# Kernel tuning notes

Hardware: AMD Instinct MI355X
Metric: run time of the kernel (lower is better)

Reference implementation:

```python
import jax, jax.numpy as jnp
import numpy as np

SEQ_LEN = 4096
EMBED_DIM = 1280
NUM_HEADS = 16
HEAD_DIM = EMBED_DIM // NUM_HEADS  # 80
SCALING = float(np.sqrt(HEAD_DIM))  # NOTE: source multiplies by sqrt(head_dim)
NEG_INF = float(np.finfo(np.float32).min)


def rotate_half(x):
    x1, x2 = jnp.split(x, 2, axis=-1)
    return jnp.concatenate((-x2, x1), axis=-1)


def setup_inputs() -> dict:
    key = jax.random.key(0)
    ks = jax.random.split(key, 7)
    s = 0.02
    hidden_states = jax.random.normal(ks[0], (SEQ_LEN, EMBED_DIM), dtype=jnp.float32)
    w_qkv = jax.random.normal(ks[1], (3 * EMBED_DIM, EMBED_DIM), dtype=jnp.float32) * s
    b_qkv = jax.random.normal(ks[2], (3 * EMBED_DIM,), dtype=jnp.float32) * s
    w_proj = jax.random.normal(ks[3], (EMBED_DIM, EMBED_DIM), dtype=jnp.float32) * s
    b_proj = jax.random.normal(ks[4], (EMBED_DIM,), dtype=jnp.float32) * s
    # rotary angles: theta duplicated to head_dim (emb = cat(rope, rope))
    inv_freq = 1.0 / (10000.0 ** (jnp.arange(0, HEAD_DIM // 2, dtype=jnp.float32) * 2.0 / HEAD_DIM))
    pos = jnp.arange(SEQ_LEN, dtype=jnp.float32)
    freqs = pos[:, None] * inv_freq[None, :]            # [S, hd/2]
    emb = jnp.concatenate((freqs, freqs), axis=-1)       # [S, hd]
    cos = jnp.cos(emb)
    sin = jnp.sin(emb)
    # 4 packed images of 1024 patches each
    cu_seqlens = jnp.array([0, 1024, 2048, 3072, 4096], dtype=jnp.int32)
    return {
        "hidden_states": hidden_states,
        "w_qkv": w_qkv, "b_qkv": b_qkv,
        "w_proj": w_proj, "b_proj": b_proj,
        "cos": cos, "sin": sin,
        "cu_seqlens": cu_seqlens,
    }


def reference(hidden_states, w_qkv, b_qkv, w_proj, b_proj, cos, sin, cu_seqlens):
    S = hidden_states.shape[0]
    # packed QKV projection
    qkv = hidden_states @ w_qkv.T + b_qkv                  # [S, 3D]
    qkv = qkv.reshape(S, 3, NUM_HEADS, HEAD_DIM)
    q, k, v = qkv[:, 0], qkv[:, 1], qkv[:, 2]              # [S, H, hd]
    # fp32 RoPE (broadcast cos/sin over heads)
    c = cos[:, None, :].astype(jnp.float32)
    sn = sin[:, None, :].astype(jnp.float32)
    qf, kf = q.astype(jnp.float32), k.astype(jnp.float32)
    q = (qf * c + rotate_half(qf) * sn).astype(q.dtype)
    k = (kf * c + rotate_half(kf) * sn).astype(k.dtype)
    # block-diagonal mask from cu_seqlens: same segment -> 0, else -inf
    pos = jnp.arange(S)
    seg = jnp.searchsorted(cu_seqlens, pos, side="right") - 1  # [S]
    bias = jnp.where(seg[:, None] == seg[None, :], 0.0, NEG_INF)  # [S, S]
    # dense attention over whole packed sequence (as in source)
    scores = jnp.einsum("shd,thd->hst", q, k) * SCALING + bias[None]
    weights = jax.nn.softmax(scores.astype(jnp.float32), axis=-1).astype(q.dtype)
    attn = jnp.einsum("hst,thd->shd", weights, v).reshape(S, EMBED_DIM)
    return attn @ w_proj.T + b_proj
```

## Files before the change

### kernel.cpp

```cpp
#include <hip/hip_runtime.h>

#define SEQ   4096
#define EMB   1280
#define NH    16
#define HD    80
#define HDP   96
#define O3    3840
#define SEGLEN 1024
#define NSEG  4
#define QSCALE (8.94427190999915878564f * 1.44269504088896340736f)

typedef unsigned short u16;
typedef __attribute__((ext_vector_type(8))) _Float16 f16x8;
typedef __attribute__((ext_vector_type(4))) _Float16 f16x4;
typedef __attribute__((ext_vector_type(2))) __fp16   h16x2;
typedef __attribute__((ext_vector_type(4))) float    f32x4;

__device__ __forceinline__ float ex2(float x) { return __builtin_amdgcn_exp2f(x); }

__device__ __forceinline__ u16 f2h(float f) {
  union { _Float16 h; u16 u; } v; v.h = (_Float16)f; return v.u;
}
__device__ __forceinline__ float h2f(u16 b) {
  union { u16 u; _Float16 h; } v; v.u = b; return (float)v.h;
}
__device__ __forceinline__ f32x4 exp2_4(f32x4 x) {
  f32x4 r; r.x = ex2(x.x); r.y = ex2(x.y); r.z = ex2(x.z); r.w = ex2(x.w); return r;
}
__device__ __forceinline__ f16x4 pk4(f32x4 s) {
  union { h16x2 h[2]; f16x4 f; } u;
  u.h[0] = __builtin_amdgcn_cvt_pkrtz(s.x, s.y);
  u.h[1] = __builtin_amdgcn_cvt_pkrtz(s.z, s.w);
  return u.f;
}
__device__ __forceinline__ void gl2lds16(const u16* g, u16* l) {
  __builtin_amdgcn_global_load_lds(
      (const __attribute__((address_space(1))) unsigned int*)g,
      (__attribute__((address_space(3))) unsigned int*)l, 16, 0, 0);
}

#define CVT_N1 (SEQ * EMB / 4)
#define CVT_N2 (O3 * EMB / 4)
#define CVT_N3 (EMB * EMB / 4)
__global__ void cvt_all_kernel(const float* __restrict__ a, const float* __restrict__ b,
                               const float* __restrict__ c, u16* __restrict__ oa,
                               u16* __restrict__ ob, u16* __restrict__ oc) {
  int i = blockIdx.x * blockDim.x + threadIdx.x;
  const float* src; u16* dst; int j = i;
  if (j < CVT_N1)                { src = a; dst = oa; }
  else if (j < CVT_N1 + CVT_N2)  { src = b; dst = ob; j -= CVT_N1; }
  else                           { src = c; dst = oc; j -= CVT_N1 + CVT_N2; }
  float4 f = ((const float4*)src)[j];
  union { u16 h[4]; uint2 v; } o;
  o.h[0] = f2h(f.x); o.h[1] = f2h(f.y); o.h[2] = f2h(f.z); o.h[3] = f2h(f.w);
  ((uint2*)dst)[j] = o.v;
}

template<int OUTF>
__global__ __launch_bounds__(256)
void gemm_bias_kernel(const u16* __restrict__ A, const u16* __restrict__ W,
                      const float* __restrict__ bias, void* __restrict__ Cout,
                      int N, int K) {
  __shared__ u16 As[128][64];
  __shared__ u16 Bs[128][64];
  const int tid  = threadIdx.x;
  const int flat = blockIdx.x + gridDim.x * blockIdx.y;
  const int cpx  = (gridDim.x * gridDim.y) >> 3;
  const int nid  = (flat & 7) * cpx + (flat >> 3);
  const int bm   = nid / gridDim.x, bn = nid % gridDim.x;
  const int lane = tid & 63;
  const int wid  = tid >> 6;
  const int wm   = (wid >> 1) * 64, wn = (wid & 1) * 64;
  const int lr   = lane & 15, quad = lane >> 4;

  f32x4 acc[4][4];
  const f32x4 z4 = {0.f, 0.f, 0.f, 0.f};
  #pragma unroll
  for (int i = 0; i < 4; ++i)
    #pragma unroll
    for (int j = 0; j < 4; ++j) acc[i][j] = z4;

  const int arow = tid >> 3;
  const int acol = (((tid & 7) ^ (arow & 7)) * 8);
  const u16* Ab = A + (size_t)(bm * 128) * K;
  const u16* Wb = W + (size_t)(bn * 128) * K;
  u16* AsL = &As[0][0] + tid * 8;
  u16* BsL = &Bs[0][0] + tid * 8;

  for (int kt = 0; kt < K; kt += 64) {
    #pragma unroll
    for (int r = 0; r < 4; ++r) {
      gl2lds16(&Ab[(size_t)(arow + r * 32) * K + kt + acol], AsL + r * 2048);
      gl2lds16(&Wb[(size_t)(arow + r * 32) * K + kt + acol], BsL + r * 2048);
    }
    __syncthreads();
    #pragma unroll
    for (int k32 = 0; k32 < 2; ++k32) {
      const int c = (((k32 * 4 + quad) ^ (lr & 7)) * 8);
      f16x8 aF[4], bF[4];
      #pragma unroll
      for (int i = 0; i < 4; ++i) {
        aF[i] = *(const f16x8*)&As[wm + i * 16 + lr][c];
        bF[i] = *(const f16x8*)&Bs[wn + i * 16 + lr][c];
      }
      #pragma unroll
      for (int i = 0; i < 4; ++i)
        #pragma unroll
        for (int j = 0; j < 4; ++j)
          acc[i][j] = __builtin_amdgcn_mfma_f32_16x16x32_f16(aF[i], bF[j], acc[i][j], 0, 0, 0);
    }
    __syncthreads();
  }

  #pragma unroll
  for (int i = 0; i < 4; ++i) {
    int rowb = bm * 128 + wm + i * 16 + quad * 4;
    #pragma unroll
    for (int j = 0; j < 4; ++j) {
      int col = bn * 128 + wn + j * 16 + lr;
      float bv = bias[col];
      #pragma unroll
      for (int r = 0; r < 4; ++r) {
        float v = acc[i][j][r] + bv;
        if (OUTF) ((float*)Cout)[(size_t)(rowb + r) * N + col] = v;
        else      ((u16*)Cout)[(size_t)(rowb + r) * N + col] = f2h(v);
      }
    }
  }
}

__global__ __launch_bounds__(512, 2)
void gemm256_kernel(const u16* __restrict__ A, const u16* __restrict__ W,
                    const float* __restrict__ bias, u16* __restrict__ Cout,
                    int N, int K) {
  __shared__ u16 As[2][256][64];
  __shared__ u16 Bs[2][256][64];
  const int tid  = threadIdx.x;
  const int flat = blockIdx.x + gridDim.x * blockIdx.y;
  const int cpx  = (gridDim.x * gridDim.y) >> 3;
  const int nid  = (flat & 7) * cpx + (flat >> 3);
  const int bm   = nid / gridDim.x, bn = nid % gridDim.x;
  const int lane = tid & 63;
  const int wid  = tid >> 6;
  const int wm   = wid >> 2;
  const int wn   = wid & 3;
  const int lr   = lane & 15, quad = lane >> 4;
  const int NT   = K >> 6;

  const u16* Ab = A + (size_t)(bm * 256) * K;
  const u16* Wb = W + (size_t)(bn * 256) * K;

  const int srr  = tid >> 3;
  const int scol = ((tid & 7) ^ (srr & 7)) << 3;
  const u16* ApL = Ab + (size_t)srr * K + scol;
  const u16* WpL = Wb + (size_t)srr * K + scol;

  auto stA = [&](int b, int row0, int t) {
    gl2lds16(ApL + (size_t)row0 * K + t * 64,        &As[b][row0][0]      + tid * 8);
    gl2lds16(ApL + (size_t)(row0 + 64) * K + t * 64, &As[b][row0 + 64][0] + tid * 8);
  };
  auto stB = [&](int b, int row0, int t) {
    gl2lds16(WpL + (size_t)row0 * K + t * 64,        &Bs[b][row0][0]      + tid * 8);
    gl2lds16(WpL + (size_t)(row0 + 64) * K + t * 64, &Bs[b][row0 + 64][0] + tid * 8);
  };

  f32x4 acc[8][4];
  const f32x4 z4 = {0.f, 0.f, 0.f, 0.f};
  #pragma unroll
  for (int i = 0; i < 8; ++i)
    #pragma unroll
    for (int j = 0; j < 4; ++j) acc[i][j] = z4;

  stA(0, 0, 0); stA(0, 128, 0);
  stB(0, 0, 0); stB(0, 128, 0);
  stA(1, 0, 1);
  asm volatile("s_waitcnt vmcnt(2)" ::: "memory");
  __builtin_amdgcn_s_barrier();

  for (int t = 0; t < NT; ++t) {
    const int buf = t & 1, nb = buf ^ 1;
    #pragma unroll
    for (int mq = 0; mq < 2; ++mq) {
      #pragma unroll
      for (int k32 = 0; k32 < 2; ++k32) {
        const int c = (((k32 * 4 + quad) ^ (lr & 7)) << 3);
        f16x8 aF[4], bF[4];
        #pragma unroll
        for (int i = 0; i < 4; ++i)
          aF[i] = *(const f16x8*)&As[buf][mq * 128 + wm * 64 + i * 16 + lr][c];
        #pragma unroll
        for (int j = 0; j < 4; ++j)
          bF[j] = *(const f16x8*)&Bs[buf][wn * 64 + j * 16 + lr][c];
        __builtin_amdgcn_sched_barrier(0);
        if (mq == 0 && k32 == 0) {
          if (t + 1 < NT) { stB(nb, 0, t + 1); stA(nb, 128, t + 1); }
        } else if (mq == 0 && k32 == 1) {
          if (t + 1 < NT) stB(nb, 128, t + 1);
        } else if (mq == 1 && k32 == 0) {
          if (t + 2 < NT) stA(buf, 0, t + 2);
        }
        __builtin_amdgcn_s_barrier();
        asm volatile("s_waitcnt lgkmcnt(0)" ::: "memory");
        __builtin_amdgcn_sched_barrier(0);
        __builtin_amdgcn_s_setprio(1);
        #pragma unroll
        for (int i = 0; i < 4; ++i)
          #pragma unroll
          for (int j = 0; j < 4; ++j)
            acc[mq * 4 + i][j] =
                __builtin_amdgcn_mfma_f32_16x16x32_f16(aF[i], bF[j], acc[mq * 4 + i][j], 0, 0, 0);
        __builtin_amdgcn_s_setprio(0);
        if (mq == 1 && k32 == 1) {
          if (t < NT - 2) asm volatile("s_waitcnt vmcnt(2)" ::: "memory");
          else            asm volatile("s_waitcnt vmcnt(0)" ::: "memory");
        }
        __builtin_amdgcn_s_barrier();
        __builtin_amdgcn_sched_barrier(0);
      }
    }
  }

  #pragma unroll
  for (int mq = 0; mq < 2; ++mq) {
    #pragma unroll
    for (int i = 0; i < 4; ++i) {
      const int rowb = bm * 256 + mq * 128 + wm * 64 + i * 16 + quad * 4;
      #pragma unroll
      for (int j = 0; j < 4; ++j) {
        const int col = bn * 256 + wn * 64 + j * 16 + lr;
        const float bv = bias[col];
        #pragma unroll
        for (int r = 0; r < 4; ++r)
          Cout[(size_t)(rowb + r) * N + col] = f2h(acc[mq * 4 + i][j][r] + bv);
      }
    }
  }
}

__global__ __launch_bounds__(256)
void rope_reorg_kernel(const u16* __restrict__ qkv, const float* __restrict__ cosp,
                       const float* __restrict__ sinp, u16* __restrict__ Qp,
                       u16* __restrict__ Kp, u16* __restrict__ Vt) {
  __shared__ u16 Qs[64][80];
  __shared__ u16 Ks[64][80];
  __shared__ u16 Vs[64][88];
  const int tid = threadIdx.x;
  const int s0 = blockIdx.x * 64;
  const int h  = blockIdx.y;

  for (int t = tid; t < 640; t += 256) {
    int r = t / 10, c = (t % 10) * 8;
    size_t g = (size_t)(s0 + r) * O3 + h * HD + c;
    *(uint4*)&Qs[r][c] = *(const uint4*)&qkv[g];
    *(uint4*)&Ks[r][c] = *(const uint4*)&qkv[g + EMB];
    *(uint4*)&Vs[r][c] = *(const uint4*)&qkv[g + 2 * EMB];
  }
  __syncthreads();

  for (int t = tid; t < 64 * 24; t += 256) {
    int r = t / 24, d4 = (t % 24) * 4;
    int s = s0 + r;
    size_t po = ((size_t)h * SEQ + s) * HDP + d4;
    if (d4 >= HD) {
      uint2 z = make_uint2(0, 0);
      *(uint2*)&Qp[po] = z; *(uint2*)&Kp[po] = z;
      continue;
    }
    float4 cv = *(const float4*)&cosp[(size_t)s * HD + d4];
    float4 sv = *(const float4*)&sinp[(size_t)s * HD + d4];
    int dp4 = (d4 < 40) ? d4 + 40 : d4 - 40;
    float sgn = (d4 < 40) ? -1.f : 1.f;
    union { u16 h[4]; uint2 v; } oq, ok;
    const float* cp = (const float*)&cv;
    const float* sp = (const float*)&sv;
    #pragma unroll
    for (int j = 0; j < 4; ++j) {
      float q  = h2f(Qs[r][d4 + j]),  k  = h2f(Ks[r][d4 + j]);
      float qp = h2f(Qs[r][dp4 + j]), kp = h2f(Ks[r][dp4 + j]);
      oq.h[j] = f2h((q * cp[j] + sgn * qp * sp[j]) * QSCALE);
      ok.h[j] = f2h(k * cp[j] + sgn * kp * sp[j]);
    }
    *(uint2*)&Qp[po] = oq.v;
    *(uint2*)&Kp[po] = ok.v;
  }

  for (int t = tid; t < HD * 8; t += 256) {
    int d = t / 8, sc = (t % 8) * 8;
    union { u16 h[8]; uint4 v; } o;
    #pragma unroll
    for (int j = 0; j < 8; ++j) o.h[j] = Vs[sc + j][d];
    *(uint4*)&Vt[((size_t)(h * HD + d)) * SEQ + s0 + sc] = o.v;
  }
}

__global__ __launch_bounds__(512)
void attn_kernel(const u16* __restrict__ Qp, const u16* __restrict__ Kp,
                 const u16* __restrict__ Vt, u16* __restrict__ attnO) {
  __shared__ u16 K_l[3][64][96];
  __shared__ u16 V_l[3][96][64];
  const int BUFSZ = 6144;

  const int tid = threadIdx.x;
  const int lane = tid & 63, w = tid >> 6;
  const int lr = lane & 15, quad = lane >> 4;
  const int flat = blockIdx.x + 8 * blockIdx.y + 128 * blockIdx.z;
  const int nid  = (flat & 7) * 64 + (flat >> 3);
  const int qb   = nid & 7;
  const int h    = (nid >> 3) & 15;
  const int sg   = nid >> 7;
  const int seg0 = sg * SEGLEN;
  const int q0b = seg0 + qb * 128;

  f16x8 qF[3];
  {
    int qrow = q0b + w * 16 + lr;
    #pragma unroll
    for (int kc = 0; kc < 3; ++kc)
      qF[kc] = *(const f16x8*)&Qp[((size_t)h * SEQ + qrow) * HDP + kc * 32 + quad * 8];
  }
  asm volatile("" :: "v"(qF[0]), "v"(qF[1]), "v"(qF[2]));
  asm volatile("s_waitcnt vmcnt(0)" ::: "memory");

  {
    u16 val = (tid < 32) ? (u16)0x3C00 : (u16)0;
    #pragma unroll
    for (int b = 0; b < 3; ++b) {
      u16* q = &V_l[0][0][0] + b * BUFSZ + 80 * 64 + tid * 2;
      q[0] = val; q[1] = val;
    }
  }

  const u16* Kbase = Kp + ((size_t)h * SEQ + seg0) * HDP;
  const u16* Vbase = Vt + (size_t)h * HD * SEQ + seg0;
  const u16* pG[3]; u16* dB[3]; int gAdv[3];
  #pragma unroll
  for (int t = 0; t < 3; ++t) {
    int s = t * 512 + tid;
    if (s < 768) {
      int r = s / 12, c = s % 12;
      int ck = (c & ~3) | ((c & 3) ^ ((r >> 1) & 3));
      pG[t] = Kbase + (size_t)r * HDP + ck * 8;
      dB[t] = &K_l[0][0][0] + s * 8;
      gAdv[t] = 64 * HDP;
    } else {
      int sv = (s < 1408) ? s - 768 : s - 1408;
      int rv = sv / 8, cv = sv % 8;
      int cg = cv ^ (rv & 7);
      pG[t] = Vbase + (size_t)rv * SEQ + cg * 8;
      dB[t] = &V_l[0][0][0] + sv * 8;
      gAdv[t] = 64;
    }
  }

  auto stage_adv = [&](int b) {
    #pragma unroll
    for (int t = 0; t < 3; ++t) {
      gl2lds16(pG[t], dB[t] + b * BUFSZ);
      pG[t] += gAdv[t];
    }
  };

  const f32x4 z4 = {0.f, 0.f, 0.f, 0.f};
  float m_r = -3.0e38f;
  f32x4 Oacc[6];
  #pragma unroll
  for (int n = 0; n < 6; ++n) Oacc[n] = z4;

  const int kswz = (lr >> 1) & 3;

  stage_adv(0);
  stage_adv(1);
  asm volatile("s_waitcnt vmcnt(3) lgkmcnt(0)" ::: "memory");
  __builtin_amdgcn_s_barrier();
  __builtin_amdgcn_sched_barrier(0);

  int buf = 0, sb = 2;
  for (int kt = 0; kt < SEGLEN; kt += 64) {
    if (kt + 128 < SEGLEN) stage_adv(sb);

    const u16* kb = &K_l[0][0][0] + buf * BUFSZ;
    const u16* vb = &V_l[0][0][0] + buf * BUFSZ;

    f32x4 S[4];
    __builtin_amdgcn_s_setprio(1);
    #pragma unroll
    for (int ct = 0; ct < 4; ++ct) {
      S[ct] = z4;
      #pragma unroll
      for (int kc = 0; kc < 3; ++kc) {
        f16x8 kF = *(const f16x8*)&kb[(ct * 16 + lr) * 96 + kc * 32 + ((quad ^ kswz) << 3)];
        S[ct] = __builtin_amdgcn_mfma_f32_16x16x32_f16(kF, qF[kc], S[ct], 0, 0, 0);
      }
    }
    __builtin_amdgcn_s_setprio(0);

    float mx = fmaxf(fmaxf(S[0].x, S[0].y), fmaxf(S[0].z, S[0].w));
    #pragma unroll
    for (int ct = 1; ct < 4; ++ct)
      mx = fmaxf(mx, fmaxf(fmaxf(S[ct].x, S[ct].y), fmaxf(S[ct].z, S[ct].w)));
    mx = fmaxf(mx, __shfl_xor(mx, 16, 64));
    mx = fmaxf(mx, __shfl_xor(mx, 32, 64));
    float mnew = fmaxf(m_r, mx);
    float alpha = ex2(m_r - mnew);
    m_r = mnew;

    f32x4 mv = {mnew, mnew, mnew, mnew};
    #pragma unroll
    for (int ct = 0; ct < 4; ++ct) S[ct] = exp2_4(S[ct] - mv);

    if (__ballot(alpha != 1.0f)) {
      f32x4 al;
      al.x = __shfl(alpha, quad * 4 + 0, 64);
      al.y = __shfl(alpha, quad * 4 + 1, 64);
      al.z = __shfl(alpha, quad * 4 + 2, 64);
      al.w = __shfl(alpha, quad * 4 + 3, 64);
      #pragma unroll
      for (int n = 0; n < 6; ++n) Oacc[n] *= al;
    }

    f16x4 pF[4];
    #pragma unroll
    for (int ct = 0; ct < 4; ++ct) pF[ct] = pk4(S[ct]);

    __builtin_amdgcn_s_setprio(1);
    #pragma unroll
    for (int ct = 0; ct < 4; ++ct) {
      const int cchunk = 2 * ct + (quad >> 1);
      #pragma unroll
      for (int n = 0; n < 6; ++n) {
        int vrow = n * 16 + lr;
        const u16* vp = vb + vrow * 64 + ((cchunk ^ (vrow & 7)) << 3) + ((quad & 1) << 2);
        f16x4 vF = *(const f16x4*)vp;
        Oacc[n] = __builtin_amdgcn_mfma_f32_16x16x16f16(pF[ct], vF, Oacc[n], 0, 0, 0);
      }
    }
    __builtin_amdgcn_s_setprio(0);

    if (kt + 128 < SEGLEN) asm volatile("s_waitcnt vmcnt(3)" ::: "memory");
    else                   asm volatile("s_waitcnt vmcnt(0)" ::: "memory");
    __builtin_amdgcn_s_barrier();
    __builtin_amdgcn_sched_barrier(0);

    buf = (buf == 2) ? 0 : buf + 1;
    sb  = (sb == 2) ? 0 : sb + 1;
  }

  f32x4 linv;
  linv.x = 1.0f / __shfl(Oacc[5].x, quad << 4, 64);
  linv.y = 1.0f / __shfl(Oacc[5].y, quad << 4, 64);
  linv.z = 1.0f / __shfl(Oacc[5].z, quad << 4, 64);
  linv.w = 1.0f / __shfl(Oacc[5].w, quad << 4, 64);
  #pragma unroll
  for (int n = 0; n < 5; ++n) {
    int rowb = q0b + w * 16 + quad * 4;
    int col = h * HD + n * 16 + lr;
    attnO[(size_t)(rowb + 0) * EMB + col] = f2h(Oacc[n].x * linv.x);
    attnO[(size_t)(rowb + 1) * EMB + col] = f2h(Oacc[n].y * linv.y);
    attnO[(size_t)(rowb + 2) * EMB + col] = f2h(Oacc[n].z * linv.z);
    attnO[(size_t)(rowb + 3) * EMB + col] = f2h(Oacc[n].w * linv.w);
  }
}

extern "C" void kernel_launch(void* const* d_in, const int* in_sizes, int n_in,
                              void* d_out, int out_size, void* d_ws, size_t ws_size,
                              hipStream_t stream) {
  const float* hs     = (const float*)d_in[0];
  const float* w_qkv  = (const float*)d_in[1];
  const float* b_qkv  = (const float*)d_in[2];
  const float* w_proj = (const float*)d_in[3];
  const float* b_proj = (const float*)d_in[4];
  const float* cosp   = (const float*)d_in[5];
  const float* sinp   = (const float*)d_in[6];
  float* out = (float*)d_out;

  char* p = (char*)d_ws;
  auto take = [&](size_t bytes) { char* q = p; p += (bytes + 255) & ~(size_t)255; return q; };
  u16* hsH    = (u16*)take((size_t)SEQ * EMB * 2);
  u16* wqkvH  = (u16*)take((size_t)O3 * EMB * 2);
  u16* wprojH = (u16*)take((size_t)EMB * EMB * 2);
  u16* qkvO   = (u16*)take((size_t)SEQ * O3 * 2);
  u16* Qp     = (u16*)take((size_t)NH * SEQ * HDP * 2);
  u16* Kp     = (u16*)take((size_t)NH * SEQ * HDP * 2);
  u16* Vt     = (u16*)take((size_t)NH * HD * SEQ * 2);
  u16* attnH  = (u16*)take((size_t)SEQ * EMB * 2);

  int ncvt = (CVT_N1 + CVT_N2 + CVT_N3) / 256;
  cvt_all_kernel<<<ncvt, 256, 0, stream>>>(hs, w_qkv, w_proj, hsH, wqkvH, wprojH);

  gemm256_kernel<<<dim3(O3 / 256, SEQ / 256), 512, 0, stream>>>(hsH, wqkvH, b_qkv, qkvO, O3, EMB);

  rope_reorg_kernel<<<dim3(SEQ / 64, NH), 256, 0, stream>>>(qkvO, cosp, sinp, Qp, Kp, Vt);

  attn_kernel<<<dim3(SEGLEN / 128, NH, NSEG), 512, 0, stream>>>(Qp, Kp, Vt, attnH);

  gemm_bias_kernel<1><<<dim3(EMB / 128, SEQ / 128), 256, 0, stream>>>(attnH, wprojH, b_proj, out, EMB, EMB);
}
```

Baseline: 233.5 us.

## Simplify GEMM pipeline to whole-tile double buffering with one barrier per K-step

```diff
diff --git a/kernel.cpp b/kernel.cpp
--- a/kernel.cpp
+++ b/kernel.cpp
@@ -155,13 +155,13 @@
   const u16* ApL = Ab + (size_t)srr * K + scol;
   const u16* WpL = Wb + (size_t)srr * K + scol;
 
-  auto stA = [&](int b, int row0, int t) {
-    gl2lds16(ApL + (size_t)row0 * K + t * 64,        &As[b][row0][0]      + tid * 8);
-    gl2lds16(ApL + (size_t)(row0 + 64) * K + t * 64, &As[b][row0 + 64][0] + tid * 8);
-  };
-  auto stB = [&](int b, int row0, int t) {
-    gl2lds16(WpL + (size_t)row0 * K + t * 64,        &Bs[b][row0][0]      + tid * 8);
-    gl2lds16(WpL + (size_t)(row0 + 64) * K + t * 64, &Bs[b][row0 + 64][0] + tid * 8);
+  auto stage = [&](int b, int t) {
+    #pragma unroll
+    for (int r = 0; r < 4; ++r)
+      gl2lds16(ApL + (size_t)(r * 64) * K + t * 64, &As[b][r * 64][0] + tid * 8);
+    #pragma unroll
+    for (int r = 0; r < 4; ++r)
+      gl2lds16(WpL + (size_t)(r * 64) * K + t * 64, &Bs[b][r * 64][0] + tid * 8);
   };
 
   f32x4 acc[8][4];
@@ -171,14 +171,17 @@
     #pragma unroll
     for (int j = 0; j < 4; ++j) acc[i][j] = z4;
 
-  stA(0, 0, 0); stA(0, 128, 0);
-  stB(0, 0, 0); stB(0, 128, 0);
-  stA(1, 0, 1);
-  asm volatile("s_waitcnt vmcnt(2)" ::: "memory");
+  stage(0, 0);
+  asm volatile("s_waitcnt vmcnt(0)" ::: "memory");
   __builtin_amdgcn_s_barrier();
+  __builtin_amdgcn_sched_barrier(0);
 
   for (int t = 0; t < NT; ++t) {
     const int buf = t & 1, nb = buf ^ 1;
+    if (t + 1 < NT) stage(nb, t + 1);
+    __builtin_amdgcn_sched_barrier(0);
+
+    __builtin_amdgcn_s_setprio(1);
     #pragma unroll
     for (int mq = 0; mq < 2; ++mq) {
       #pragma unroll
@@ -191,33 +194,19 @@
         #pragma unroll
         for (int j = 0; j < 4; ++j)
           bF[j] = *(const f16x8*)&Bs[buf][wn * 64 + j * 16 + lr][c];
-        __builtin_amdgcn_sched_barrier(0);
-        if (mq == 0 && k32 == 0) {
-          if (t + 1 < NT) { stB(nb, 0, t + 1); stA(nb, 128, t + 1); }
-        } else if (mq == 0 && k32 == 1) {
-          if (t + 1 < NT) stB(nb, 128, t + 1);
-        } else if (mq == 1 && k32 == 0) {
-          if (t + 2 < NT) stA(buf, 0, t + 2);
-        }
-        __builtin_amdgcn_s_barrier();
-        asm volatile("s_waitcnt lgkmcnt(0)" ::: "memory");
-        __builtin_amdgcn_sched_barrier(0);
-        __builtin_amdgcn_s_setprio(1);
         #pragma unroll
         for (int i = 0; i < 4; ++i)
           #pragma unroll
           for (int j = 0; j < 4; ++j)
             acc[mq * 4 + i][j] =
                 __builtin_amdgcn_mfma_f32_16x16x32_f16(aF[i], bF[j], acc[mq * 4 + i][j], 0, 0, 0);
-        __builtin_amdgcn_s_setprio(0);
-        if (mq == 1 && k32 == 1) {
-          if (t < NT - 2) asm volatile("s_waitcnt vmcnt(2)" ::: "memory");
-          else            asm volatile("s_waitcnt vmcnt(0)" ::: "memory");
-        }
-        __builtin_amdgcn_s_barrier();
-        __builtin_amdgcn_sched_barrier(0);
-      }
-    }
+      }
+    }
+    __builtin_amdgcn_s_setprio(0);
+
+    asm volatile("s_waitcnt vmcnt(0)" ::: "memory");
+    __builtin_amdgcn_s_barrier();
+    __builtin_amdgcn_sched_barrier(0);
   }
 
   #pragma unroll
```

After: 234.6 us. No clear change (+0.5%).

## Restructure GEMM k-loop into two phases with fewer barriers and shared B fragments

Applied to the files above, without the earlier changes.

```diff
diff --git a/kernel.cpp b/kernel.cpp
--- a/kernel.cpp
+++ b/kernel.cpp
@@ -171,53 +171,67 @@
     #pragma unroll
     for (int j = 0; j < 4; ++j) acc[i][j] = z4;
 
+  const int c0 = (((0 * 4 + quad) ^ (lr & 7)) << 3);
+  const int c1 = (((1 * 4 + quad) ^ (lr & 7)) << 3);
+
   stA(0, 0, 0); stA(0, 128, 0);
   stB(0, 0, 0); stB(0, 128, 0);
   stA(1, 0, 1);
   asm volatile("s_waitcnt vmcnt(2)" ::: "memory");
   __builtin_amdgcn_s_barrier();
+  __builtin_amdgcn_sched_barrier(0);
 
   for (int t = 0; t < NT; ++t) {
     const int buf = t & 1, nb = buf ^ 1;
-    #pragma unroll
-    for (int mq = 0; mq < 2; ++mq) {
-      #pragma unroll
-      for (int k32 = 0; k32 < 2; ++k32) {
-        const int c = (((k32 * 4 + quad) ^ (lr & 7)) << 3);
-        f16x8 aF[4], bF[4];
-        #pragma unroll
-        for (int i = 0; i < 4; ++i)
-          aF[i] = *(const f16x8*)&As[buf][mq * 128 + wm * 64 + i * 16 + lr][c];
+
+    f16x8 bF[2][4], aF0[2][4];
+    #pragma unroll
+    for (int j = 0; j < 4; ++j) {
+      bF[0][j] = *(const f16x8*)&Bs[buf][wn * 64 + j * 16 + lr][c0];
+      bF[1][j] = *(const f16x8*)&Bs[buf][wn * 64 + j * 16 + lr][c1];
+    }
+    #pragma unroll
+    for (int i = 0; i < 4; ++i) {
+      aF0[0][i] = *(const f16x8*)&As[buf][wm * 64 + i * 16 + lr][c0];
+      aF0[1][i] = *(const f16x8*)&As[buf][wm * 64 + i * 16 + lr][c1];
+    }
+    __builtin_amdgcn_sched_barrier(0);
+    if (t + 1 < NT) { stB(nb, 0, t + 1); stB(nb, 128, t + 1); stA(nb, 128, t + 1); }
+    __builtin_amdgcn_sched_barrier(0);
+    __builtin_amdgcn_s_setprio(1);
+    #pragma unroll
+    for (int k32 = 0; k32 < 2; ++k32)
+      #pragma unroll
+      for (int i = 0; i < 4; ++i)
         #pragma unroll
         for (int j = 0; j < 4; ++j)
-          bF[j] = *(const f16x8*)&Bs[buf][wn * 64 + j * 16 + lr][c];
-        __builtin_amdgcn_sched_barrier(0);
-        if (mq == 0 && k32 == 0) {
-          if (t + 1 < NT) { stB(nb, 0, t + 1); stA(nb, 128, t + 1); }
-        } else if (mq == 0 && k32 == 1) {
-          if (t + 1 < NT) stB(nb, 128, t + 1);
-        } else if (mq == 1 && k32 == 0) {
-          if (t + 2 < NT) stA(buf, 0, t + 2);
-        }
-        __builtin_amdgcn_s_barrier();
-        asm volatile("s_waitcnt lgkmcnt(0)" ::: "memory");
-        __builtin_amdgcn_sched_barrier(0);
-        __builtin_amdgcn_s_setprio(1);
+          acc[i][j] = __builtin_amdgcn_mfma_f32_16x16x32_f16(aF0[k32][i], bF[k32][j], acc[i][j], 0, 0, 0);
+    __builtin_amdgcn_s_setprio(0);
+    __builtin_amdgcn_sched_barrier(0);
+    __builtin_amdgcn_s_barrier();
+
+    f16x8 aF1[2][4];
+    #pragma unroll
+    for (int i = 0; i < 4; ++i) {
+      aF1[0][i] = *(const f16x8*)&As[buf][128 + wm * 64 + i * 16 + lr][c0];
+      aF1[1][i] = *(const f16x8*)&As[buf][128 + wm * 64 + i * 16 + lr][c1];
+    }
+    __builtin_amdgcn_sched_barrier(0);
+    if (t + 2 < NT) stA(buf, 0, t + 2);
+    __builtin_amdgcn_sched_barrier(0);
+    __builtin_amdgcn_s_setprio(1);
+    #pragma unroll
+    for (int k32 = 0; k32 < 2; ++k32)
+      #pragma unroll
+      for (int i = 0; i < 4; ++i)
         #pragma unroll
-        for (int i = 0; i < 4; ++i)
-          #pragma unroll
-          for (int j = 0; j < 4; ++j)
-            acc[mq * 4 + i][j] =
-                __builtin_amdgcn_mfma_f32_16x16x32_f16(aF[i], bF[j], acc[mq * 4 + i][j], 0, 0, 0);
-        __builtin_amdgcn_s_setprio(0);
-        if (mq == 1 && k32 == 1) {
-          if (t < NT - 2) asm volatile("s_waitcnt vmcnt(2)" ::: "memory");
-          else            asm volatile("s_waitcnt vmcnt(0)" ::: "memory");
-        }
-        __builtin_amdgcn_s_barrier();
-        __builtin_amdgcn_sched_barrier(0);
-      }
-    }
+        for (int j = 0; j < 4; ++j)
+          acc[4 + i][j] = __builtin_amdgcn_mfma_f32_16x16x32_f16(aF1[k32][i], bF[k32][j], acc[4 + i][j], 0, 0, 0);
+    __builtin_amdgcn_s_setprio(0);
+    if (t < NT - 2) asm volatile("s_waitcnt vmcnt(2)" ::: "memory");
+    else            asm volatile("s_waitcnt vmcnt(0)" ::: "memory");
+    __builtin_amdgcn_s_barrier();
+    __builtin_amdgcn_sched_barrier(0);
   }
 
   #pragma unroll
```

Measured after the change: 225.3 us. 1.04x faster.
